# Optimization experiments

Hardware: AMD Instinct MI355X
Metric: run time of the kernel (lower is better)

Reference implementation:

```python
import jax, jax.numpy as jnp
import numpy as np

ALPHA = 0.2        # LeakyReLU slope
NEG_BIG = -9e15    # mask fill value from the original module


def setup_inputs() -> dict:
    key = jax.random.key(0)
    k1, k2, k3, k4 = jax.random.split(key, 4)
    N, F_IN, F_OUT = 8192, 256, 128
    h = jax.random.normal(k1, (N, F_IN), dtype=jnp.float32)
    adj = jax.random.randint(k2, (N, N), 0, 2, dtype=jnp.int32)
    W = jax.random.normal(k3, (F_IN, F_OUT), dtype=jnp.float32) * (1.0 / np.sqrt(F_IN))
    a = jax.random.normal(k4, (2 * F_OUT, 1), dtype=jnp.float32) * (1.0 / np.sqrt(2 * F_OUT))
    return {"h": h, "adj": adj, "W": W, "a": a}


def reference(h, adj, W, a):
    f_out = W.shape[1]
    Wh = h @ W                                   # [N, F_out]
    Wh1 = Wh @ a[:f_out, :]                      # [N, 1]
    Wh2 = Wh @ a[f_out:, :]                      # [N, 1]
    e = Wh1 + Wh2.T                              # [N, N] broadcast-add
    e = jnp.where(e > 0, e, ALPHA * e)           # LeakyReLU
    e = jnp.where(adj > 0, e, NEG_BIG)           # adjacency mask
    attention = jax.nn.softmax(e, axis=-1)       # row softmax
    # dropout rate = 0.0 -> identity
    h_prime = attention @ Wh                     # [N, F_out]
    return jax.nn.elu(h_prime)
```

## Files before the change

### kernel.cpp

```cpp
#include <hip/hip_runtime.h>

#define NV 8192
#define FIN 256
#define FOUT 128
#define SPLITS 8
#define PANEL 1024

typedef __bf16 bf16_t;
typedef __attribute__((ext_vector_type(8))) __bf16 bf16x8;
typedef __attribute__((ext_vector_type(16))) float f32x16;

__global__ __launch_bounds__(256) void wh_kernel(
    const float* __restrict__ h, const float* __restrict__ W,
    const float* __restrict__ a,
    bf16_t* __restrict__ WhbT, float* __restrict__ Wh1, float* __restrict__ Wh2)
{
  __shared__ float As[64][34];
  __shared__ float Bs[64][128];
  __shared__ float Cs[32][129];
  __shared__ float red1[32][16];
  __shared__ float red2[32][16];
  const int t  = threadIdx.x;
  const int i0 = blockIdx.x * 32;
  const int c  = t & 15;
  const int r  = t >> 4;
  float acc0[8], acc1[8];
  #pragma unroll
  for (int j = 0; j < 8; j++) { acc0[j] = 0.f; acc1[j] = 0.f; }

  for (int k0 = 0; k0 < FIN; k0 += 64) {
    {
      const int ia = t >> 3;
      const int ka = (t & 7) * 8;
      const float* src = h + (size_t)(i0 + ia) * FIN + k0 + ka;
      float4 v0 = *(const float4*)src;
      float4 v1 = *(const float4*)(src + 4);
      As[ka+0][ia]=v0.x; As[ka+1][ia]=v0.y; As[ka+2][ia]=v0.z; As[ka+3][ia]=v0.w;
      As[ka+4][ia]=v1.x; As[ka+5][ia]=v1.y; As[ka+6][ia]=v1.z; As[ka+7][ia]=v1.w;
    }
    {
      const int kb = t >> 2;
      const int cb = (t & 3) * 32;
      const float4* src = (const float4*)(W + (size_t)(k0 + kb) * FOUT + cb);
      float4* dst = (float4*)&Bs[kb][cb];
      #pragma unroll
      for (int q = 0; q < 8; q++) dst[q] = src[q];
    }
    __syncthreads();
    #pragma unroll 4
    for (int k = 0; k < 64; k++) {
      float2 av = *(const float2*)&As[k][r*2];
      float b[8];
      *(float4*)&b[0] = *(const float4*)&Bs[k][c*8];
      *(float4*)&b[4] = *(const float4*)&Bs[k][c*8+4];
      #pragma unroll
      for (int j = 0; j < 8; j++) {
        acc0[j] = fmaf(av.x, b[j], acc0[j]);
        acc1[j] = fmaf(av.y, b[j], acc1[j]);
      }
    }
    __syncthreads();
  }

  float p1a = 0.f, p2a = 0.f, p1b = 0.f, p2b = 0.f;
  #pragma unroll
  for (int j = 0; j < 8; j++) {
    Cs[r*2][c*8+j]   = acc0[j];
    Cs[r*2+1][c*8+j] = acc1[j];
    float w1 = a[c*8+j];
    float w2 = a[FOUT + c*8+j];
    p1a = fmaf(acc0[j], w1, p1a); p2a = fmaf(acc0[j], w2, p2a);
    p1b = fmaf(acc1[j], w1, p1b); p2b = fmaf(acc1[j], w2, p2b);
  }
  red1[r*2][c]   = p1a; red2[r*2][c]   = p2a;
  red1[r*2+1][c] = p1b; red2[r*2+1][c] = p2b;
  __syncthreads();
  if (t < 32) {
    float s = 0.f;
    #pragma unroll
    for (int q = 0; q < 16; q++) s += red1[t][q];
    Wh1[i0 + t] = s;
  } else if (t < 64) {
    float s = 0.f;
    #pragma unroll
    for (int q = 0; q < 16; q++) s += red2[t-32][q];
    Wh2[i0 + t - 32] = s;
  }
  {
    const int f = t & 127, half = t >> 7;
    union { bf16_t b[16]; uint4 v[2]; } pk;
    #pragma unroll
    for (int q = 0; q < 16; q++) pk.b[q] = (bf16_t)Cs[half*16 + q][f];
    uint4* dst = (uint4*)(WhbT + (size_t)f * NV + i0 + half*16);
    dst[0] = pk.v[0]; dst[1] = pk.v[1];
  }
}

#define LOAD8(buf, off) do {                                                  \
    _Pragma("unroll")                                                         \
    for (int ks = 0; ks < 4; ks++) {                                          \
      buf[ks*2]   = *(const int4*)(rowp + (off) + ks*16 + hi8);               \
      buf[ks*2+1] = *(const int4*)(rowp + (off) + ks*16 + hi8 + 4);           \
    } } while (0)

#define PROCESS(buf, jc) do {                                                 \
    const int jbL = j0 + (jc);                                                \
    bf16x8 af[4];                                                             \
    _Pragma("unroll")                                                         \
    for (int ks = 0; ks < 4; ks++) {                                          \
      float4 wA = *(const float4*)(Wh2v + jbL + ks*16 + hi8);                 \
      float4 wB = *(const float4*)(Wh2v + jbL + ks*16 + hi8 + 4);             \
      const float wm[8] = {wA.x,wA.y,wA.z,wA.w, wB.x,wB.y,wB.z,wB.w};         \
      const int4 aa = buf[ks*2], ab = buf[ks*2+1];                            \
      const int am[8] = {aa.x,aa.y,aa.z,aa.w, ab.x,ab.y,ab.z,ab.w};           \
      _Pragma("unroll")                                                       \
      for (int q = 0; q < 8; q++) {                                           \
        float e = wh1 + wm[q];                                                \
        e = fmaxf(e, 0.2f * e);                           \
        float p = (am[q] > 0) ? __expf(e) : 0.0f;             \
        den_t += p;                                                           \
        af[ks][q] = (bf16_t)p;                                                \
      }                                                                       \
    }                                                                         \
    _Pragma("unroll")                                                         \
    for (int nb = 0; nb < 4; nb++) {                                          \
      _Pragma("unroll")                                                       \
      for (int ks = 0; ks < 4; ks++) {                                        \
        bf16x8 bfv = *(const bf16x8*)(bp + (size_t)(nb*32 + ml) * NV          \
                                      + (jc) + ks*16 + hi8);                  \
        acc[nb] = __builtin_amdgcn_mfma_f32_32x32x16_bf16(af[ks], bfv,        \
                                                          acc[nb], 0, 0, 0); \
      }                                                                       \
    } } while (0)

__global__ __launch_bounds__(256, 2) void attn_kernel(
    const int* __restrict__ adj, const bf16_t* __restrict__ WhbT,
    const float* __restrict__ Wh1v, const float* __restrict__ Wh2v,
    float* __restrict__ nump, float* __restrict__ denp)
{
  const int t     = threadIdx.x;
  const int lane  = t & 63;
  const int w     = t >> 6;
  const int ml    = lane & 31;
  const int hi    = lane >> 5;
  const int hi8   = hi * 8;
  const int rb    = blockIdx.x >> 3;
  const int split = blockIdx.x & 7;
  const int i0    = rb * 128;
  const int j0    = split * PANEL;
  const int row   = i0 + w * 32 + ml;
  const float wh1 = Wh1v[row];
  const int* rowp = adj + (size_t)row * NV + j0;
  const bf16_t* bp = WhbT + j0;
  f32x16 acc[4] = {};
  float den_t = 0.f;
  int4 c0[8], c1[8];

  LOAD8(c0, 0);
  #pragma unroll 1
  for (int jc = 0; jc < PANEL; jc += 128) {
    LOAD8(c1, jc + 64);
    PROCESS(c0, jc);
    const int off2 = (jc + 128 < PANEL) ? jc + 128 : 0;
    LOAD8(c0, off2);
    PROCESS(c1, jc + 64);
  }

  den_t += __shfl(den_t, lane ^ 32, 64);
  if (hi == 0) denp[(size_t)split * NV + row] = den_t;

  float* base = nump + ((size_t)split * NV + i0 + w * 32) * FOUT;
  const int r4 = 4 * hi;
  #pragma unroll
  for (int nb = 0; nb < 4; nb++) {
    #pragma unroll
    for (int reg = 0; reg < 16; reg++) {
      const int crow = (reg & 3) + 8 * (reg >> 2) + r4;
      base[(size_t)crow * FOUT + nb * 32 + ml] = acc[nb][reg];
    }
  }
}

__global__ __launch_bounds__(256) void finalize_kernel(
    const float* __restrict__ nump, const float* __restrict__ denp,
    float* __restrict__ out)
{
  const int gid = blockIdx.x * 256 + threadIdx.x;
  const int i  = gid >> 5;
  const int f0 = (gid & 31) * 4;
  float den = 0.f;
  #pragma unroll
  for (int s = 0; s < SPLITS; s++) den += denp[(size_t)s * NV + i];
  float4 sv = make_float4(0.f, 0.f, 0.f, 0.f);
  #pragma unroll
  for (int s = 0; s < SPLITS; s++) {
    float4 v = *(const float4*)&nump[((size_t)s * NV + i) * FOUT + f0];
    sv.x += v.x; sv.y += v.y; sv.z += v.z; sv.w += v.w;
  }
  const float inv = 1.0f / den;
  float4 r;
  r.x = sv.x * inv; r.y = sv.y * inv; r.z = sv.z * inv; r.w = sv.w * inv;
  r.x = r.x > 0.f ? r.x : __expf(r.x) - 1.0f;
  r.y = r.y > 0.f ? r.y : __expf(r.y) - 1.0f;
  r.z = r.z > 0.f ? r.z : __expf(r.z) - 1.0f;
  r.w = r.w > 0.f ? r.w : __expf(r.w) - 1.0f;
  *(float4*)&out[(size_t)i * FOUT + f0] = r;
}

extern "C" void kernel_launch(void* const* d_in, const int* in_sizes, int n_in,
                              void* d_out, int out_size, void* d_ws, size_t ws_size,
                              hipStream_t stream) {
  const float* h  = (const float*)d_in[0];
  const int*  adj = (const int*)d_in[1];
  const float* W  = (const float*)d_in[2];
  const float* a  = (const float*)d_in[3];
  float* out = (float*)d_out;
  char* ws = (char*)d_ws;
  bf16_t* WhbT = (bf16_t*)ws;
  float* Wh1  = (float*)(ws + 2097152);
  float* Wh2  = (float*)(ws + 2097152 + 32768);
  float* denp = (float*)(ws + 2097152 + 65536);
  float* nump = (float*)(ws + 2097152 + 65536 + 262144);

  wh_kernel<<<256, 256, 0, stream>>>(h, W, a, WhbT, Wh1, Wh2);
  attn_kernel<<<512, 256, 0, stream>>>(adj, WhbT, Wh1, Wh2, nump, denp);
  finalize_kernel<<<1024, 256, 0, stream>>>(nump, denp, out);
}
```

Measured before the change: 477.3 us.

## Switch attention to 16x16x32 MFMA with pre-swizzled Wh layout and LDS Wh2

Replaces the 32x32x16 MFMA tiling with 16x16x32 MFMA: each wave now handles 16 rows across all 128 output features, and row blocks shrink to 64 so the grid doubles to 1024 blocks. wh_kernel writes Wh in a fragment-swizzled bf16 layout, so B operands load as contiguous 16-byte lanes instead of strided rows of a transposed matrix. Wh2 for the panel is staged in LDS, and sched_barriers place the next adjacency prefetch after the B loads. The aim is better coalescing of B loads, more occupancy (launch bounds raised to 3 blocks), and better overlap of adj streaming. The cost is more B-operand traffic per row, since fewer rows share each Wh fetch.

```diff
diff --git a/kernel.cpp b/kernel.cpp
--- a/kernel.cpp
+++ b/kernel.cpp
@@ -8,12 +8,12 @@
 
 typedef __bf16 bf16_t;
 typedef __attribute__((ext_vector_type(8))) __bf16 bf16x8;
-typedef __attribute__((ext_vector_type(16))) float f32x16;
+typedef __attribute__((ext_vector_type(4))) float f32x4;
 
 __global__ __launch_bounds__(256) void wh_kernel(
     const float* __restrict__ h, const float* __restrict__ W,
     const float* __restrict__ a,
-    bf16_t* __restrict__ WhbT, float* __restrict__ Wh1, float* __restrict__ Wh2)
+    bf16_t* __restrict__ Wg, float* __restrict__ Wh1, float* __restrict__ Wh2)
 {
   __shared__ float As[64][34];
   __shared__ float Bs[64][128];
@@ -88,95 +88,112 @@
   }
   {
     const int f = t & 127, half = t >> 7;
-    union { bf16_t b[16]; uint4 v[2]; } pk;
-    #pragma unroll
-    for (int q = 0; q < 16; q++) pk.b[q] = (bf16_t)Cs[half*16 + q][f];
-    uint4* dst = (uint4*)(WhbT + (size_t)f * NV + i0 + half*16);
-    dst[0] = pk.v[0]; dst[1] = pk.v[1];
-  }
-}
-
-#define LOAD8(buf, off) do {                                                  \
+    const int fb = f >> 4, f15 = f & 15;
+    union { bf16_t b[8]; uint4 v; } p0, p1;
+    #pragma unroll
+    for (int q = 0; q < 8; q++) {
+      p0.b[q] = (bf16_t)Cs[half*16 + q][f];
+      p1.b[q] = (bf16_t)Cs[half*16 + 8 + q][f];
+    }
+    size_t base = (size_t)(i0 >> 5) * 4096 + (size_t)fb * 512
+                + (size_t)(2*half) * 128 + (size_t)f15 * 8;
+    *(uint4*)(Wg + base)       = p0.v;
+    *(uint4*)(Wg + base + 128) = p1.v;
+  }
+}
+
+#define LOADC(buf, jc) do {                                                   \
+    buf[0] = *(const int4*)(rowp + (jc));                                     \
+    buf[1] = *(const int4*)(rowp + (jc) + 4);                                 \
+    buf[2] = *(const int4*)(rowp + (jc) + 32);                                \
+    buf[3] = *(const int4*)(rowp + (jc) + 32 + 4);                            \
+  } while (0)
+
+#define PCOMP(buf, jc, s, af) do {                                            \
+    const int4 aa = buf[(s)*2], ab = buf[(s)*2+1];                            \
+    const int am[8] = {aa.x,aa.y,aa.z,aa.w, ab.x,ab.y,ab.z,ab.w};             \
+    float4 wA = *(const float4*)&Wh2s[(jc) + (s)*32 + kh8];                   \
+    float4 wB = *(const float4*)&Wh2s[(jc) + (s)*32 + kh8 + 4];               \
+    const float wm[8] = {wA.x,wA.y,wA.z,wA.w, wB.x,wB.y,wB.z,wB.w};           \
     _Pragma("unroll")                                                         \
-    for (int ks = 0; ks < 4; ks++) {                                          \
-      buf[ks*2]   = *(const int4*)(rowp + (off) + ks*16 + hi8);               \
-      buf[ks*2+1] = *(const int4*)(rowp + (off) + ks*16 + hi8 + 4);           \
+    for (int q = 0; q < 8; q++) {                                             \
+      float e = wh1 + wm[q];                                                  \
+      e = fmaxf(e, 0.2f * e);                             \
+      float p = (am[q] > 0) ? __expf(e) : 0.0f;               \
+      den_t += p;                                                             \
+      af[q] = (bf16_t)p;                                                      \
     } } while (0)
 
-#define PROCESS(buf, jc) do {                                                 \
-    const int jbL = j0 + (jc);                                                \
-    bf16x8 af[4];                                                             \
+#define BODY(BUF, JC, NBUF, NJC) do {                                         \
+    bf16x8 af0, af1;                                                          \
+    PCOMP(BUF, (JC), 0, af0);                                                 \
+    PCOMP(BUF, (JC), 1, af1);                                                 \
+    const bf16_t* bb0 = Wg + (size_t)((j0 + (JC)) >> 5) * 4096 + lane8;       \
+    const bf16_t* bb1 = Wg + (size_t)((j0 + (JC) + 32) >> 5) * 4096 + lane8;  \
+    bf16x8 b0[8], b1[8];                                                      \
     _Pragma("unroll")                                                         \
-    for (int ks = 0; ks < 4; ks++) {                                          \
-      float4 wA = *(const float4*)(Wh2v + jbL + ks*16 + hi8);                 \
-      float4 wB = *(const float4*)(Wh2v + jbL + ks*16 + hi8 + 4);             \
-      const float wm[8] = {wA.x,wA.y,wA.z,wA.w, wB.x,wB.y,wB.z,wB.w};         \
-      const int4 aa = buf[ks*2], ab = buf[ks*2+1];                            \
-      const int am[8] = {aa.x,aa.y,aa.z,aa.w, ab.x,ab.y,ab.z,ab.w};           \
-      _Pragma("unroll")                                                       \
-      for (int q = 0; q < 8; q++) {                                           \
-        float e = wh1 + wm[q];                                                \
-        e = fmaxf(e, 0.2f * e);                           \
-        float p = (am[q] > 0) ? __expf(e) : 0.0f;             \
-        den_t += p;                                                           \
-        af[ks][q] = (bf16_t)p;                                                \
-      }                                                                       \
+    for (int fb = 0; fb < 8; fb++) {                                          \
+      b0[fb] = *(const bf16x8*)(bb0 + fb * 512);                              \
+      b1[fb] = *(const bf16x8*)(bb1 + fb * 512);                              \
     }                                                                         \
+    __builtin_amdgcn_sched_barrier(0);                                        \
+    LOADC(NBUF, (NJC));                                                       \
+    __builtin_amdgcn_sched_barrier(0);                                        \
     _Pragma("unroll")                                                         \
-    for (int nb = 0; nb < 4; nb++) {                                          \
-      _Pragma("unroll")                                                       \
-      for (int ks = 0; ks < 4; ks++) {                                        \
-        bf16x8 bfv = *(const bf16x8*)(bp + (size_t)(nb*32 + ml) * NV          \
-                                      + (jc) + ks*16 + hi8);                  \
-        acc[nb] = __builtin_amdgcn_mfma_f32_32x32x16_bf16(af[ks], bfv,        \
-                                                          acc[nb], 0, 0, 0); \
-      }                                                                       \
+    for (int fb = 0; fb < 8; fb++) {                                          \
+      acc[fb] = __builtin_amdgcn_mfma_f32_16x16x32_bf16(af0, b0[fb],          \
+                                                        acc[fb], 0, 0, 0);    \
+      acc[fb] = __builtin_amdgcn_mfma_f32_16x16x32_bf16(af1, b1[fb],          \
+                                                        acc[fb], 0, 0, 0);    \
     } } while (0)
 
-__global__ __launch_bounds__(256, 2) void attn_kernel(
-    const int* __restrict__ adj, const bf16_t* __restrict__ WhbT,
+__global__ __launch_bounds__(256, 3) void attn_kernel(
+    const int* __restrict__ adj, const bf16_t* __restrict__ Wg,
     const float* __restrict__ Wh1v, const float* __restrict__ Wh2v,
     float* __restrict__ nump, float* __restrict__ denp)
 {
+  __shared__ float Wh2s[PANEL];
   const int t     = threadIdx.x;
   const int lane  = t & 63;
   const int w     = t >> 6;
-  const int ml    = lane & 31;
-  const int hi    = lane >> 5;
-  const int hi8   = hi * 8;
+  const int f15   = lane & 15;
+  const int kh    = lane >> 4;
+  const int kh8   = kh * 8;
+  const int lane8 = lane * 8;
   const int rb    = blockIdx.x >> 3;
   const int split = blockIdx.x & 7;
-  const int i0    = rb * 128;
+  const int i0    = rb * 64;
   const int j0    = split * PANEL;
-  const int row   = i0 + w * 32 + ml;
+  const int row   = i0 + w * 16 + f15;
   const float wh1 = Wh1v[row];
-  const int* rowp = adj + (size_t)row * NV + j0;
-  const bf16_t* bp = WhbT + j0;
-  f32x16 acc[4] = {};
+  const int* rowp = adj + (size_t)row * NV + j0 + kh8;
+
+  *(float4*)&Wh2s[t * 4] = *(const float4*)(Wh2v + j0 + t * 4);
+  __syncthreads();
+
+  f32x4 acc[8] = {};
   float den_t = 0.f;
-  int4 c0[8], c1[8];
-
-  LOAD8(c0, 0);
+  int4 c0[4], c1[4];
+
+  LOADC(c0, 0);
   #pragma unroll 1
   for (int jc = 0; jc < PANEL; jc += 128) {
-    LOAD8(c1, jc + 64);
-    PROCESS(c0, jc);
-    const int off2 = (jc + 128 < PANEL) ? jc + 128 : 0;
-    LOAD8(c0, off2);
-    PROCESS(c1, jc + 64);
-  }
-
-  den_t += __shfl(den_t, lane ^ 32, 64);
-  if (hi == 0) denp[(size_t)split * NV + row] = den_t;
-
-  float* base = nump + ((size_t)split * NV + i0 + w * 32) * FOUT;
-  const int r4 = 4 * hi;
-  #pragma unroll
-  for (int nb = 0; nb < 4; nb++) {
-    #pragma unroll
-    for (int reg = 0; reg < 16; reg++) {
-      const int crow = (reg & 3) + 8 * (reg >> 2) + r4;
-      base[(size_t)crow * FOUT + nb * 32 + ml] = acc[nb][reg];
+    BODY(c0, jc, c1, jc + 64);
+    const int njc = (jc + 128 < PANEL) ? jc + 128 : 0;
+    BODY(c1, jc + 64, c0, njc);
+  }
+
+  den_t += __shfl_xor(den_t, 16, 64);
+  den_t += __shfl_xor(den_t, 32, 64);
+  if (lane < 16) denp[(size_t)split * NV + i0 + w * 16 + lane] = den_t;
+
+  float* base = nump + ((size_t)split * NV + i0 + w * 16) * FOUT;
+  #pragma unroll
+  for (int fb = 0; fb < 8; fb++) {
+    #pragma unroll
+    for (int reg = 0; reg < 4; reg++) {
+      const int crow = kh * 4 + reg;
+      base[(size_t)crow * FOUT + fb * 16 + f15] = acc[fb][reg];
     }
   }
 }
@@ -216,13 +233,13 @@
   const float* a  = (const float*)d_in[3];
   float* out = (float*)d_out;
   char* ws = (char*)d_ws;
-  bf16_t* WhbT = (bf16_t*)ws;
+  bf16_t* Wg  = (bf16_t*)ws;
   float* Wh1  = (float*)(ws + 2097152);
   float* Wh2  = (float*)(ws + 2097152 + 32768);
   float* denp = (float*)(ws + 2097152 + 65536);
   float* nump = (float*)(ws + 2097152 + 65536 + 262144);
 
-  wh_kernel<<<256, 256, 0, stream>>>(h, W, a, WhbT, Wh1, Wh2);
-  attn_kernel<<<512, 256, 0, stream>>>(adj, WhbT, Wh1, Wh2, nump, denp);
+  wh_kernel<<<256, 256, 0, stream>>>(h, W, a, Wg, Wh1, Wh2);
+  attn_kernel<<<1024, 256, 0, stream>>>(adj, Wg, Wh1, Wh2, nump, denp);
   finalize_kernel<<<1024, 256, 0, stream>>>(nump, denp, out);
 }
```

Measured after the change: 425.0 us. 1.12x faster.
